# Performance work log

Hardware: AMD Instinct MI355X
Metric: run time of the kernel (lower is better)

Reference implementation:

```python
import jax, jax.numpy as jnp
import numpy as np

N = 25000      # nodes
E = 200000     # edges (avg degree 8)
DIN = 512      # input_dim
HID = 512      # hidden_dim


def setup_inputs() -> dict:
    key = jax.random.key(0)
    ks = jax.random.split(key, 8)
    x = jax.random.normal(ks[0], (N, DIN), jnp.float32)
    edge_index = jax.random.randint(ks[1], (2, E), 0, N, jnp.int32)
    s_in = 1.0 / np.sqrt(DIN).astype(np.float32)
    s_h = 1.0 / np.sqrt(HID).astype(np.float32)
    W1 = jax.random.normal(ks[2], (DIN, HID), jnp.float32) * s_in
    b1 = jnp.zeros((HID,), jnp.float32)
    W2 = jax.random.normal(ks[3], (HID, HID), jnp.float32) * s_h
    b2 = jnp.zeros((HID,), jnp.float32)
    Wo = jax.random.normal(ks[4], (HID, 1), jnp.float32) * s_h
    bo = jnp.zeros((1,), jnp.float32)
    Ww = jax.random.normal(ks[5], (HID, 1), jnp.float32) * s_h
    bw = jnp.zeros((1,), jnp.float32)
    return dict(x=x, edge_index=edge_index, W1=W1, b1=b1, W2=W2, b2=b2,
                Wo=Wo, bo=bo, Ww=Ww, bw=bw)


def reference(x, edge_index, W1, b1, W2, b2, Wo, bo, Ww, bw):
    n = x.shape[0]
    src, dst = edge_index[0], edge_index[1]
    # GCNConv with self-loops: deg counts incoming edges + 1 self-loop
    deg = jax.ops.segment_sum(jnp.ones(src.shape[0], x.dtype), dst,
                              num_segments=n) + 1.0
    dis = jax.lax.rsqrt(deg)              # deg^{-1/2}, [N]
    norm = dis[src] * dis[dst]            # per-edge symmetric norm, [E]

    def gcn(h, W, b):
        hw = h @ W                        # [N, H] dense GEMM
        msg = hw[src] * norm[:, None]     # gather + scale, [E, H]
        agg = jax.ops.segment_sum(msg, dst, num_segments=n)
        agg = agg + hw * (dis * dis)[:, None]  # self-loop contribution
        return agg + b

    h1 = jax.nn.relu(gcn(x, W1, b1))
    h2 = jax.nn.relu(gcn(h1, W2, b2))
    open_logits = (h2 @ Wo + bo)[:, 0]
    wall_logits = (h2 @ Ww + bw)[:, 0]
    return open_logits, wall_logits
```

## Files before the change

kernel.cpp:

```cpp
#include <hip/hip_runtime.h>
#include <hip/hip_bf16.h>

#define DIN 512
#define HID 512

#define AS1 __attribute__((address_space(1)))
#define AS3 __attribute__((address_space(3)))

typedef __attribute__((ext_vector_type(8))) short bfrag;
typedef __attribute__((ext_vector_type(4))) float ffrag;
typedef __attribute__((ext_vector_type(8))) unsigned short u16x8;
typedef __attribute__((ext_vector_type(4))) unsigned short u16x4;

__global__ __launch_bounds__(256) void prelude(const float* __restrict__ x,
                                               unsigned short* __restrict__ xb,
                                               const float* __restrict__ W1,
                                               const float* __restrict__ W2,
                                               unsigned short* __restrict__ Wt1,
                                               unsigned short* __restrict__ Wt2,
                                               const int* __restrict__ dst,
                                               int* __restrict__ cnt,
                                               int E, int Nvalid, int C1) {
    int b = blockIdx.x;
    if (b < C1) {
        int idx = b * 256 + threadIdx.x;
        int row = idx >> 6;
        int c = (idx & 63) * 8;
        unsigned short o[8];
        if (row < Nvalid) {
            float4 a = *(const float4*)&x[(size_t)row * 512 + c];
            float4 v = *(const float4*)&x[(size_t)row * 512 + c + 4];
            __hip_bfloat16 t;
            t = __float2bfloat16(a.x); o[0] = *(unsigned short*)&t;
            t = __float2bfloat16(a.y); o[1] = *(unsigned short*)&t;
            t = __float2bfloat16(a.z); o[2] = *(unsigned short*)&t;
            t = __float2bfloat16(a.w); o[3] = *(unsigned short*)&t;
            t = __float2bfloat16(v.x); o[4] = *(unsigned short*)&t;
            t = __float2bfloat16(v.y); o[5] = *(unsigned short*)&t;
            t = __float2bfloat16(v.z); o[6] = *(unsigned short*)&t;
            t = __float2bfloat16(v.w); o[7] = *(unsigned short*)&t;
        } else {
#pragma unroll
            for (int j = 0; j < 8; ++j) o[j] = 0;
        }
        *(u16x8*)&xb[(size_t)row * 512 + c] = *(u16x8*)o;
    } else if (b < C1 + 512) {
        int bb = b - C1;
        int which = bb >> 8;
        bb &= 255;
        const float* W = which ? W2 : W1;
        unsigned short* Wt = which ? Wt2 : Wt1;
        __shared__ float t[32][33];
        int tid = threadIdx.x;
        int tx = tid & 31, ty = tid >> 5;
        int n0 = (bb & 15) * 32, k0 = (bb >> 4) * 32;
#pragma unroll
        for (int s = 0; s < 4; ++s)
            t[ty + 8 * s][tx] = W[(size_t)(k0 + ty + 8 * s) * 512 + n0 + tx];
        __syncthreads();
#pragma unroll
        for (int s = 0; s < 4; ++s) {
            __hip_bfloat16 v = __float2bfloat16(t[tx][ty + 8 * s]);
            Wt[(size_t)(n0 + ty + 8 * s) * 512 + k0 + tx] = *(unsigned short*)&v;
        }
    } else {
        int e = (b - C1 - 512) * 256 + threadIdx.x;
        if (e < E) atomicAdd(&cnt[dst[e]], 1);
    }
}

__global__ __launch_bounds__(256) void scan1(const int* __restrict__ cnt, int* __restrict__ tmp,
                                             int* __restrict__ bsum, int N) {
    int tid = threadIdx.x, lane = tid & 63, wave = tid >> 6;
    int i = blockIdx.x * 256 + tid;
    int v = (i < N) ? cnt[i] : 0;
    int incl = v;
#pragma unroll
    for (int o = 1; o < 64; o <<= 1) {
        int t = __shfl_up(incl, o);
        if (lane >= o) incl += t;
    }
    __shared__ int wtot[4];
    if (lane == 63) wtot[wave] = incl;
    __syncthreads();
    int woff = 0;
#pragma unroll
    for (int w = 0; w < 4; ++w) woff += (w < wave) ? wtot[w] : 0;
    if (i < N) tmp[i] = woff + incl - v;
    if (tid == 255) bsum[blockIdx.x] = woff + incl;
}

__global__ void scan2(int* __restrict__ bsum, int nb) {
    int tid = threadIdx.x;
    int lane = tid & 63, wave = tid >> 6;
    int v = (tid < nb) ? bsum[tid] : 0;
    int incl = v;
#pragma unroll
    for (int o = 1; o < 64; o <<= 1) {
        int t = __shfl_up(incl, o);
        if (lane >= o) incl += t;
    }
    __shared__ int w0;
    if (tid == 63) w0 = incl;
    __syncthreads();
    int off = wave ? w0 : 0;
    if (tid < nb) bsum[tid] = off + incl - v;
    if (tid == 127) bsum[nb] = off + incl;
}

__global__ void scan3(const int* __restrict__ cnt, const int* __restrict__ tmp,
                      const int* __restrict__ bsum, int* __restrict__ offs,
                      int* __restrict__ cursor, float* __restrict__ dis,
                      float* __restrict__ out, const float* __restrict__ bo,
                      const float* __restrict__ bw, int N, int nb) {
    int i = blockIdx.x * 256 + threadIdx.x;
    if (i < N) {
        int o = tmp[i] + bsum[i >> 8];
        offs[i] = o;
        cursor[i] = o;
        dis[i] = rsqrtf((float)cnt[i] + 1.0f);
        out[i] = bo[0];
        out[N + i] = bw[0];
    }
    if (i == 0) offs[N] = bsum[nb];
}

__global__ void fill_kernel(const int* __restrict__ src, const int* __restrict__ dst,
                            int* __restrict__ cursor, const float* __restrict__ dis,
                            int2* __restrict__ csr2, int E) {
    int e = blockIdx.x * 256 + threadIdx.x;
    if (e >= E) return;
    int d = dst[e];
    int s = src[e];
    int pos = atomicAdd(&cursor[d], 1);
    int2 rec;
    rec.x = s;
    rec.y = __float_as_int(dis[s]);
    csr2[pos] = rec;
}

__device__ inline bool tile_map(int b, int Mtiles, int& m0, int& n0) {
    int xcd = b & 7, i = b >> 3;
    int nt = i & 3, mg = i >> 2;
    int mt = mg * 8 + xcd;
    if (mt >= Mtiles) return false;
    m0 = mt * 128;
    n0 = nt * 128;
    return true;
}

__global__ __launch_bounds__(256) void gemm_bf16(const short* __restrict__ A,
                                                 const short* __restrict__ B,
                                                 unsigned short* __restrict__ C,
                                                 int Mtiles) {
    __shared__ __align__(16) short As[128 * 64];
    __shared__ __align__(16) short Bs[128 * 64];
    const int K = 512;
    int m0, n0;
    if (!tile_map(blockIdx.x, Mtiles, m0, n0)) return;
    int tid = threadIdx.x;
    int lane = tid & 63, wave = tid >> 6;
    int wm = (wave & 1) * 64;
    int wn = (wave >> 1) * 64;
    int r = lane & 15, q = lane >> 4;

    unsigned aoff[4], boff[4]; int ldso[4];
#pragma unroll
    for (int i = 0; i < 4; ++i) {
        int s = i * 256 + tid;
        int row = s >> 3;
        int c = (s & 7) ^ (row & 7);
        aoff[i] = (unsigned)(m0 + row) * K + c * 8;
        boff[i] = (unsigned)(n0 + row) * K + c * 8;
        ldso[i] = (i * 256 + (tid & ~63)) * 8;
    }

    ffrag acc[4][4];
#pragma unroll
    for (int i = 0; i < 4; ++i)
#pragma unroll
        for (int j = 0; j < 4; ++j) acc[i][j] = ffrag{0.f, 0.f, 0.f, 0.f};

    for (int k0 = 0; k0 < K; k0 += 64) {
#pragma unroll
        for (int i = 0; i < 4; ++i) {
            __builtin_amdgcn_global_load_lds((const AS1 void*)(A + aoff[i] + k0),
                                             (AS3 void*)(As + ldso[i]), 16, 0, 0);
            __builtin_amdgcn_global_load_lds((const AS1 void*)(B + boff[i] + k0),
                                             (AS3 void*)(Bs + ldso[i]), 16, 0, 0);
        }
        __syncthreads();

#pragma unroll
        for (int s2 = 0; s2 < 2; ++s2) {
            bfrag af[4], bfr[4];
#pragma unroll
            for (int i = 0; i < 4; ++i) {
                int arow = wm + i * 16 + r;
                int ach = (s2 * 4 + q) ^ (arow & 7);
                af[i] = *(const bfrag*)&As[arow * 64 + ach * 8];
                int brow = wn + i * 16 + r;
                int bch = (s2 * 4 + q) ^ (brow & 7);
                bfr[i] = *(const bfrag*)&Bs[brow * 64 + bch * 8];
            }
#pragma unroll
            for (int i = 0; i < 4; ++i)
#pragma unroll
                for (int j = 0; j < 4; ++j)
                    acc[i][j] = __builtin_amdgcn_mfma_f32_16x16x32_bf16(bfr[j], af[i], acc[i][j], 0, 0, 0);
        }
        __syncthreads();
    }

#pragma unroll
    for (int i = 0; i < 4; ++i) {
        int m = m0 + wm + i * 16 + r;
#pragma unroll
        for (int j = 0; j < 4; ++j) {
            int n = n0 + wn + j * 16 + q * 4;
            u16x4 o;
#pragma unroll
            for (int reg = 0; reg < 4; ++reg) {
                __hip_bfloat16 v = __float2bfloat16(acc[i][j][reg]);
                o[reg] = *(unsigned short*)&v;
            }
            *(u16x4*)&C[(size_t)m * 512 + n] = o;
        }
    }
}

__device__ inline void cvt8(u16x8 v, float* f) {
#pragma unroll
    for (int j = 0; j < 8; ++j) f[j] = __uint_as_float((unsigned)v[j] << 16);
}

__global__ __launch_bounds__(256) void agg_relu_sh(const unsigned short* __restrict__ hw,
                                                   const int2* __restrict__ csr2,
                                                   const int* __restrict__ offs,
                                                   const float* __restrict__ dis,
                                                   const float* __restrict__ bias,
                                                   unsigned short* __restrict__ out,
                                                   int N, int Mpad) {
    int b = blockIdx.x;
    int shard = b & 7;
    int tid = threadIdx.x;
    int wave = tid >> 6, lane = tid & 63;
    int cluster = lane >> 3;
    int sub = lane & 7;
    int node = (b >> 3) * 32 + wave * 8 + cluster;
    int c0 = shard * 64 + sub * 8;
    if (node >= N) {
        if (node < Mpad) {
            u16x8 z = {0, 0, 0, 0, 0, 0, 0, 0};
            *(u16x8*)&out[(size_t)node * HID + c0] = z;
        }
        return;
    }

    float dn = dis[node];
    int e0 = offs[node], e1 = offs[node + 1];

    float acc[8];
    {
        u16x8 sv = *(const u16x8*)&hw[(size_t)node * HID + c0];
        float g[8];
        cvt8(sv, g);
        float4 bb0 = *(const float4*)&bias[c0];
        float4 bb1 = *(const float4*)&bias[c0 + 4];
        float dis2 = dn * dn;
        acc[0] = g[0] * dis2 + bb0.x; acc[1] = g[1] * dis2 + bb0.y;
        acc[2] = g[2] * dis2 + bb0.z; acc[3] = g[3] * dis2 + bb0.w;
        acc[4] = g[4] * dis2 + bb1.x; acc[5] = g[5] * dis2 + bb1.y;
        acc[6] = g[6] * dis2 + bb1.z; acc[7] = g[7] * dis2 + bb1.w;
    }

    for (int e = e0; e < e1; e += 4) {
        int idx[4]; float wgt[4];
#pragma unroll
        for (int j = 0; j < 4; ++j) {
            int ee = e + j;
            int ec = (ee < e1) ? ee : (e1 - 1);
            int2 rec = csr2[ec];
            idx[j] = rec.x;
            wgt[j] = (ee < e1) ? __int_as_float(rec.y) * dn : 0.f;
        }
        u16x8 v[4];
#pragma unroll
        for (int j = 0; j < 4; ++j)
            v[j] = *(const u16x8*)&hw[(size_t)idx[j] * HID + c0];
#pragma unroll
        for (int j = 0; j < 4; ++j) {
            float g[8];
            cvt8(v[j], g);
#pragma unroll
            for (int t = 0; t < 8; ++t) acc[t] += g[t] * wgt[j];
        }
    }

    unsigned short o[8];
#pragma unroll
    for (int j = 0; j < 8; ++j) {
        __hip_bfloat16 v = __float2bfloat16(fmaxf(acc[j], 0.f));
        o[j] = *(unsigned short*)&v;
    }
    *(u16x8*)&out[(size_t)node * HID + c0] = *(u16x8*)o;
}

__global__ __launch_bounds__(256) void agg_heads_sh(const unsigned short* __restrict__ hw,
                                                    const int2* __restrict__ csr2,
                                                    const int* __restrict__ offs,
                                                    const float* __restrict__ dis,
                                                    const float* __restrict__ bias,
                                                    const float* __restrict__ Wo,
                                                    const float* __restrict__ Ww,
                                                    float* __restrict__ out, int N) {
    int b = blockIdx.x;
    int shard = b & 7;
    int tid = threadIdx.x;
    int wave = tid >> 6, lane = tid & 63;
    int cluster = lane >> 3;
    int sub = lane & 7;
    int node = (b >> 3) * 32 + wave * 8 + cluster;
    if (node >= N) return;
    int c0 = shard * 64 + sub * 8;

    float dn = dis[node];
    int e0 = offs[node], e1 = offs[node + 1];

    float acc[8];
    {
        u16x8 sv = *(const u16x8*)&hw[(size_t)node * HID + c0];
        float g[8];
        cvt8(sv, g);
        float4 bb0 = *(const float4*)&bias[c0];
        float4 bb1 = *(const float4*)&bias[c0 + 4];
        float dis2 = dn * dn;
        acc[0] = g[0] * dis2 + bb0.x; acc[1] = g[1] * dis2 + bb0.y;
        acc[2] = g[2] * dis2 + bb0.z; acc[3] = g[3] * dis2 + bb0.w;
        acc[4] = g[4] * dis2 + bb1.x; acc[5] = g[5] * dis2 + bb1.y;
        acc[6] = g[6] * dis2 + bb1.z; acc[7] = g[7] * dis2 + bb1.w;
    }

    for (int e = e0; e < e1; e += 4) {
        int idx[4]; float wgt[4];
#pragma unroll
        for (int j = 0; j < 4; ++j) {
            int ee = e + j;
            int ec = (ee < e1) ? ee : (e1 - 1);
            int2 rec = csr2[ec];
            idx[j] = rec.x;
            wgt[j] = (ee < e1) ? __int_as_float(rec.y) * dn : 0.f;
        }
        u16x8 v[4];
#pragma unroll
        for (int j = 0; j < 4; ++j)
            v[j] = *(const u16x8*)&hw[(size_t)idx[j] * HID + c0];
#pragma unroll
        for (int j = 0; j < 4; ++j) {
            float g[8];
            cvt8(v[j], g);
#pragma unroll
            for (int t = 0; t < 8; ++t) acc[t] += g[t] * wgt[j];
        }
    }

    float4 wo0 = *(const float4*)&Wo[c0];
    float4 wo1 = *(const float4*)&Wo[c0 + 4];
    float4 ww0 = *(const float4*)&Ww[c0];
    float4 ww1 = *(const float4*)&Ww[c0 + 4];
    float po = 0.f, pw = 0.f, h;
    h = fmaxf(acc[0], 0.f); po += h * wo0.x; pw += h * ww0.x;
    h = fmaxf(acc[1], 0.f); po += h * wo0.y; pw += h * ww0.y;
    h = fmaxf(acc[2], 0.f); po += h * wo0.z; pw += h * ww0.z;
    h = fmaxf(acc[3], 0.f); po += h * wo0.w; pw += h * ww0.w;
    h = fmaxf(acc[4], 0.f); po += h * wo1.x; pw += h * ww1.x;
    h = fmaxf(acc[5], 0.f); po += h * wo1.y; pw += h * ww1.y;
    h = fmaxf(acc[6], 0.f); po += h * wo1.z; pw += h * ww1.z;
    h = fmaxf(acc[7], 0.f); po += h * wo1.w; pw += h * ww1.w;

#pragma unroll
    for (int off = 4; off > 0; off >>= 1) {
        po += __shfl_down(po, off);
        pw += __shfl_down(pw, off);
    }
    if (sub == 0) {
        atomicAdd(&out[node], po);
        atomicAdd(&out[N + node], pw);
    }
}

extern "C" void kernel_launch(void* const* d_in, const int* in_sizes, int n_in,
                              void* d_out, int out_size, void* d_ws, size_t ws_size,
                              hipStream_t stream) {
    const float* x  = (const float*)d_in[0];
    const int*   ei = (const int*)d_in[1];
    const float* W1 = (const float*)d_in[2];
    const float* b1 = (const float*)d_in[3];
    const float* W2 = (const float*)d_in[4];
    const float* b2 = (const float*)d_in[5];
    const float* Wo = (const float*)d_in[6];
    const float* bo = (const float*)d_in[7];
    const float* Ww = (const float*)d_in[8];
    const float* bw = (const float*)d_in[9];

    const int N = in_sizes[0] / DIN;
    const int E = in_sizes[1] / 2;
    const int Mpad = (N + 127) & ~127;
    const int Mtiles = Mpad / 128;
    const int nb = (N + 255) / 256;
    const int C1 = Mpad / 4;

    char* ws = (char*)d_ws;
    size_t p = 0;
    auto alloc = [&](size_t bytes) -> char* {
        char* r = ws + p;
        p += (bytes + 255) & ~(size_t)255;
        return r;
    };
    int*   cnt    = (int*)alloc((size_t)N * 4);
    int*   offs   = (int*)alloc((size_t)(N + 1) * 4);
    int*   cursor = (int*)alloc((size_t)N * 4);
    int*   tmp    = (int*)alloc((size_t)N * 4);
    int*   bsum   = (int*)alloc(132 * 4);
    float* dis    = (float*)alloc((size_t)N * 4);
    int2*  csr2   = (int2*)alloc((size_t)E * 8 + 64);
    unsigned short* xb  = (unsigned short*)alloc((size_t)Mpad * 512 * 2);
    unsigned short* Wt1 = (unsigned short*)alloc((size_t)512 * 512 * 2);
    unsigned short* Wt2 = (unsigned short*)alloc((size_t)512 * 512 * 2);
    unsigned short* hw  = (unsigned short*)alloc((size_t)Mpad * 512 * 2);
    unsigned short* h1  = (unsigned short*)alloc((size_t)Mpad * 512 * 2);

    const int* src = ei;
    const int* dst = ei + E;

    hipMemsetAsync(cnt, 0, (size_t)N * 4, stream);

    prelude<<<C1 + 512 + (E + 255) / 256, 256, 0, stream>>>(x, xb, W1, W2, Wt1, Wt2,
                                                            dst, cnt, E, N, C1);
    scan1<<<nb, 256, 0, stream>>>(cnt, tmp, bsum, N);
    scan2<<<1, 128, 0, stream>>>(bsum, nb);
    scan3<<<nb, 256, 0, stream>>>(cnt, tmp, bsum, offs, cursor, dis,
                                  (float*)d_out, bo, bw, N, nb);
    fill_kernel<<<(E + 255) / 256, 256, 0, stream>>>(src, dst, cursor, dis, csr2, E);

    const int ggrid = 8 * ((Mtiles + 7) / 8) * 4;
    gemm_bf16<<<ggrid, 256, 0, stream>>>((const short*)xb, (const short*)Wt1, hw, Mtiles);
    agg_relu_sh<<<8 * (Mpad / 32), 256, 0, stream>>>(hw, csr2, offs, dis, b1, h1, N, Mpad);
    gemm_bf16<<<ggrid, 256, 0, stream>>>((const short*)h1, (const short*)Wt2, hw, Mtiles);
    agg_heads_sh<<<8 * ((N + 31) / 32), 256, 0, stream>>>(hw, csr2, offs, dis, b2,
                                                          Wo, Ww, (float*)d_out, N);
}
```

Measured before the change: 247.2 us.

## Replace prefix scan with atomic offset assignment and degree-sorted node permutation

Drops the three-kernel prefix scan. Each node now takes its CSR offset from a single global atomic counter, so segments are no longer laid out in node order, and segment ends come from the degree rather than offs[node+1]. It also bucket-sorts nodes by degree into a permutation, so the aggregation kernels process nodes of similar degree together and the 8 nodes in a wave see less load imbalance. The costs are heavy contention on one global atomic, less locality in the CSR layout, and indirect node indexing through perm in the aggregation kernels.

```diff
diff --git a/kernel.cpp b/kernel.cpp
--- a/kernel.cpp
+++ b/kernel.cpp
@@ -69,74 +69,62 @@
     }
 }
 
-__global__ __launch_bounds__(256) void scan1(const int* __restrict__ cnt, int* __restrict__ tmp,
-                                             int* __restrict__ bsum, int N) {
-    int tid = threadIdx.x, lane = tid & 63, wave = tid >> 6;
-    int i = blockIdx.x * 256 + tid;
-    int v = (i < N) ? cnt[i] : 0;
-    int incl = v;
-#pragma unroll
-    for (int o = 1; o < 64; o <<= 1) {
-        int t = __shfl_up(incl, o);
-        if (lane >= o) incl += t;
-    }
-    __shared__ int wtot[4];
-    if (lane == 63) wtot[wave] = incl;
-    __syncthreads();
-    int woff = 0;
-#pragma unroll
-    for (int w = 0; w < 4; ++w) woff += (w < wave) ? wtot[w] : 0;
-    if (i < N) tmp[i] = woff + incl - v;
-    if (tid == 255) bsum[blockIdx.x] = woff + incl;
-}
-
-__global__ void scan2(int* __restrict__ bsum, int nb) {
-    int tid = threadIdx.x;
-    int lane = tid & 63, wave = tid >> 6;
-    int v = (tid < nb) ? bsum[tid] : 0;
-    int incl = v;
-#pragma unroll
-    for (int o = 1; o < 64; o <<= 1) {
-        int t = __shfl_up(incl, o);
-        if (lane >= o) incl += t;
-    }
-    __shared__ int w0;
-    if (tid == 63) w0 = incl;
-    __syncthreads();
-    int off = wave ? w0 : 0;
-    if (tid < nb) bsum[tid] = off + incl - v;
-    if (tid == 127) bsum[nb] = off + incl;
-}
-
-__global__ void scan3(const int* __restrict__ cnt, const int* __restrict__ tmp,
-                      const int* __restrict__ bsum, int* __restrict__ offs,
-                      int* __restrict__ cursor, float* __restrict__ dis,
-                      float* __restrict__ out, const float* __restrict__ bo,
-                      const float* __restrict__ bw, int N, int nb) {
+__global__ __launch_bounds__(256) void assign(int* __restrict__ cnt,
+                                              int* __restrict__ offs,
+                                              int* __restrict__ cursor,
+                                              float* __restrict__ dis,
+                                              float* __restrict__ out,
+                                              const float* __restrict__ bo,
+                                              const float* __restrict__ bw,
+                                              int N) {
+    int* bcnt = cnt + N;
+    int* gctr = cnt + N + 128;
     int i = blockIdx.x * 256 + threadIdx.x;
-    if (i < N) {
-        int o = tmp[i] + bsum[i >> 8];
-        offs[i] = o;
-        cursor[i] = o;
-        dis[i] = rsqrtf((float)cnt[i] + 1.0f);
-        out[i] = bo[0];
-        out[N + i] = bw[0];
-    }
-    if (i == 0) offs[N] = bsum[nb];
-}
-
-__global__ void fill_kernel(const int* __restrict__ src, const int* __restrict__ dst,
-                            int* __restrict__ cursor, const float* __restrict__ dis,
-                            int2* __restrict__ csr2, int E) {
-    int e = blockIdx.x * 256 + threadIdx.x;
-    if (e >= E) return;
-    int d = dst[e];
-    int s = src[e];
-    int pos = atomicAdd(&cursor[d], 1);
-    int2 rec;
-    rec.x = s;
-    rec.y = __float_as_int(dis[s]);
-    csr2[pos] = rec;
+    if (i >= N) return;
+    int d = cnt[i];
+    int o = atomicAdd(gctr, d);
+    offs[i] = o;
+    cursor[i] = o;
+    dis[i] = rsqrtf((float)d + 1.0f);
+    out[i] = bo[0];
+    out[N + i] = bw[0];
+    int b = (d < 63) ? d : 63;
+    atomicAdd(&bcnt[b], 1);
+}
+
+__global__ __launch_bounds__(256) void fill2(const int* __restrict__ src,
+                                             const int* __restrict__ dst,
+                                             int* __restrict__ cursor,
+                                             const float* __restrict__ dis,
+                                             int2* __restrict__ csr2,
+                                             int* __restrict__ cnt,
+                                             int* __restrict__ perm,
+                                             int E, int N, int EJ) {
+    int b = blockIdx.x;
+    if (b < EJ) {
+        int e = b * 256 + threadIdx.x;
+        if (e >= E) return;
+        int d = dst[e];
+        int s = src[e];
+        int pos = atomicAdd(&cursor[d], 1);
+        int2 rec;
+        rec.x = s;
+        rec.y = __float_as_int(dis[s]);
+        csr2[pos] = rec;
+    } else {
+        const int* bcnt = cnt + N;
+        int* bcur = cnt + N + 64;
+        int i = (b - EJ) * 256 + threadIdx.x;
+        if (i >= N) return;
+        int d = cnt[i];
+        int myb = (d < 63) ? d : 63;
+        int base = 0;
+#pragma unroll
+        for (int k = 0; k < 63; ++k)
+            base += (k < myb) ? bcnt[k] : 0;
+        int p = atomicAdd(&bcur[myb], 1);
+        perm[base + p] = i;
+    }
 }
 
 __device__ inline bool tile_map(int b, int Mtiles, int& m0, int& n0) {
@@ -237,8 +225,10 @@
 __global__ __launch_bounds__(256) void agg_relu_sh(const unsigned short* __restrict__ hw,
                                                    const int2* __restrict__ csr2,
                                                    const int* __restrict__ offs,
+                                                   const int* __restrict__ deg,
                                                    const float* __restrict__ dis,
                                                    const float* __restrict__ bias,
+                                                   const int* __restrict__ perm,
                                                    unsigned short* __restrict__ out,
                                                    int N, int Mpad) {
     int b = blockIdx.x;
@@ -247,18 +237,19 @@
     int wave = tid >> 6, lane = tid & 63;
     int cluster = lane >> 3;
     int sub = lane & 7;
-    int node = (b >> 3) * 32 + wave * 8 + cluster;
+    int j = (b >> 3) * 32 + wave * 8 + cluster;
     int c0 = shard * 64 + sub * 8;
-    if (node >= N) {
-        if (node < Mpad) {
+    if (j >= N) {
+        if (j < Mpad) {
             u16x8 z = {0, 0, 0, 0, 0, 0, 0, 0};
-            *(u16x8*)&out[(size_t)node * HID + c0] = z;
+            *(u16x8*)&out[(size_t)j * HID + c0] = z;
         }
         return;
     }
+    int node = perm[j];
 
     float dn = dis[node];
-    int e0 = offs[node], e1 = offs[node + 1];
+    int e0 = offs[node], e1 = e0 + deg[node];
 
     float acc[8];
     {
@@ -277,31 +268,31 @@
     for (int e = e0; e < e1; e += 4) {
         int idx[4]; float wgt[4];
 #pragma unroll
-        for (int j = 0; j < 4; ++j) {
-            int ee = e + j;
+        for (int t = 0; t < 4; ++t) {
+            int ee = e + t;
             int ec = (ee < e1) ? ee : (e1 - 1);
             int2 rec = csr2[ec];
-            idx[j] = rec.x;
-            wgt[j] = (ee < e1) ? __int_as_float(rec.y) * dn : 0.f;
+            idx[t] = rec.x;
+            wgt[t] = (ee < e1) ? __int_as_float(rec.y) * dn : 0.f;
         }
         u16x8 v[4];
 #pragma unroll
-        for (int j = 0; j < 4; ++j)
-            v[j] = *(const u16x8*)&hw[(size_t)idx[j] * HID + c0];
-#pragma unroll
-        for (int j = 0; j < 4; ++j) {
+        for (int t = 0; t < 4; ++t)
+            v[t] = *(const u16x8*)&hw[(size_t)idx[t] * HID + c0];
+#pragma unroll
+        for (int t = 0; t < 4; ++t) {
             float g[8];
-            cvt8(v[j], g);
-#pragma unroll
-            for (int t = 0; t < 8; ++t) acc[t] += g[t] * wgt[j];
+            cvt8(v[t], g);
+#pragma unroll
+            for (int u = 0; u < 8; ++u) acc[u] += g[u] * wgt[t];
         }
     }
 
     unsigned short o[8];
 #pragma unroll
-    for (int j = 0; j < 8; ++j) {
-        __hip_bfloat16 v = __float2bfloat16(fmaxf(acc[j], 0.f));
-        o[j] = *(unsigned short*)&v;
+    for (int t = 0; t < 8; ++t) {
+        __hip_bfloat16 v = __float2bfloat16(fmaxf(acc[t], 0.f));
+        o[t] = *(unsigned short*)&v;
     }
     *(u16x8*)&out[(size_t)node * HID + c0] = *(u16x8*)o;
 }
@@ -309,10 +300,12 @@
 __global__ __launch_bounds__(256) void agg_heads_sh(const unsigned short* __restrict__ hw,
                                                     const int2* __restrict__ csr2,
                                                     const int* __restrict__ offs,
+                                                    const int* __restrict__ deg,
                                                     const float* __restrict__ dis,
                                                     const float* __restrict__ bias,
                                                     const float* __restrict__ Wo,
                                                     const float* __restrict__ Ww,
+                                                    const int* __restrict__ perm,
                                                     float* __restrict__ out, int N) {
     int b = blockIdx.x;
     int shard = b & 7;
@@ -320,12 +313,13 @@
     int wave = tid >> 6, lane = tid & 63;
     int cluster = lane >> 3;
     int sub = lane & 7;
-    int node = (b >> 3) * 32 + wave * 8 + cluster;
-    if (node >= N) return;
+    int j = (b >> 3) * 32 + wave * 8 + cluster;
+    if (j >= N) return;
+    int node = perm[j];
     int c0 = shard * 64 + sub * 8;
 
     float dn = dis[node];
-    int e0 = offs[node], e1 = offs[node + 1];
+    int e0 = offs[node], e1 = e0 + deg[node];
 
     float acc[8];
     {
@@ -344,23 +338,23 @@
     for (int e = e0; e < e1; e += 4) {
         int idx[4]; float wgt[4];
 #pragma unroll
-        for (int j = 0; j < 4; ++j) {
-            int ee = e + j;
+        for (int t = 0; t < 4; ++t) {
+            int ee = e + t;
             int ec = (ee < e1) ? ee : (e1 - 1);
             int2 rec = csr2[ec];
-            idx[j] = rec.x;
-            wgt[j] = (ee < e1) ? __int_as_float(rec.y) * dn : 0.f;
+            idx[t] = rec.x;
+            wgt[t] = (ee < e1) ? __int_as_float(rec.y) * dn : 0.f;
         }
         u16x8 v[4];
 #pragma unroll
-        for (int j = 0; j < 4; ++j)
-            v[j] = *(const u16x8*)&hw[(size_t)idx[j] * HID + c0];
-#pragma unroll
-        for (int j = 0; j < 4; ++j) {
+        for (int t = 0; t < 4; ++t)
+            v[t] = *(const u16x8*)&hw[(size_t)idx[t] * HID + c0];
+#pragma unroll
+        for (int t = 0; t < 4; ++t) {
             float g[8];
-            cvt8(v[j], g);
-#pragma unroll
-            for (int t = 0; t < 8; ++t) acc[t] += g[t] * wgt[j];
+            cvt8(v[t], g);
+#pragma unroll
+            for (int u = 0; u < 8; ++u) acc[u] += g[u] * wgt[t];
         }
     }
 
@@ -409,6 +403,7 @@
     const int Mtiles = Mpad / 128;
     const int nb = (N + 255) / 256;
     const int C1 = Mpad / 4;
+    const int EJ = (E + 255) / 256;
 
     char* ws = (char*)d_ws;
     size_t p = 0;
@@ -417,11 +412,10 @@
         p += (bytes + 255) & ~(size_t)255;
         return r;
     };
-    int*   cnt    = (int*)alloc((size_t)N * 4);
-    int*   offs   = (int*)alloc((size_t)(N + 1) * 4);
+    int*   cnt    = (int*)alloc((size_t)(N + 132) * 4);
+    int*   offs   = (int*)alloc((size_t)N * 4);
     int*   cursor = (int*)alloc((size_t)N * 4);
-    int*   tmp    = (int*)alloc((size_t)N * 4);
-    int*   bsum   = (int*)alloc(132 * 4);
+    int*   perm   = (int*)alloc((size_t)N * 4);
     float* dis    = (float*)alloc((size_t)N * 4);
     int2*  csr2   = (int2*)alloc((size_t)E * 8 + 64);
     unsigned short* xb  = (unsigned short*)alloc((size_t)Mpad * 512 * 2);
@@ -433,20 +427,20 @@
     const int* src = ei;
     const int* dst = ei + E;
 
-    hipMemsetAsync(cnt, 0, (size_t)N * 4, stream);
-
-    prelude<<<C1 + 512 + (E + 255) / 256, 256, 0, stream>>>(x, xb, W1, W2, Wt1, Wt2,
-                                                            dst, cnt, E, N, C1);
-    scan1<<<nb, 256, 0, stream>>>(cnt, tmp, bsum, N);
-    scan2<<<1, 128, 0, stream>>>(bsum, nb);
-    scan3<<<nb, 256, 0, stream>>>(cnt, tmp, bsum, offs, cursor, dis,
-                                  (float*)d_out, bo, bw, N, nb);
-    fill_kernel<<<(E + 255) / 256, 256, 0, stream>>>(src, dst, cursor, dis, csr2, E);
+    hipMemsetAsync(cnt, 0, (size_t)(N + 132) * 4, stream);
+
+    prelude<<<C1 + 512 + EJ, 256, 0, stream>>>(x, xb, W1, W2, Wt1, Wt2,
+                                               dst, cnt, E, N, C1);
+    assign<<<nb, 256, 0, stream>>>(cnt, offs, cursor, dis,
+                                   (float*)d_out, bo, bw, N);
+    fill2<<<EJ + nb, 256, 0, stream>>>(src, dst, cursor, dis, csr2, cnt, perm,
+                                       E, N, EJ);
 
     const int ggrid = 8 * ((Mtiles + 7) / 8) * 4;
     gemm_bf16<<<ggrid, 256, 0, stream>>>((const short*)xb, (const short*)Wt1, hw, Mtiles);
-    agg_relu_sh<<<8 * (Mpad / 32), 256, 0, stream>>>(hw, csr2, offs, dis, b1, h1, N, Mpad);
+    agg_relu_sh<<<8 * (Mpad / 32), 256, 0, stream>>>(hw, csr2, offs, cnt, dis, b1,
+                                                     perm, h1, N, Mpad);
     gemm_bf16<<<ggrid, 256, 0, stream>>>((const short*)h1, (const short*)Wt2, hw, Mtiles);
-    agg_heads_sh<<<8 * ((N + 31) / 32), 256, 0, stream>>>(hw, csr2, offs, dis, b2,
-                                                          Wo, Ww, (float*)d_out, N);
-}
+    agg_heads_sh<<<8 * ((N + 31) / 32), 256, 0, stream>>>(hw, csr2, offs, cnt, dis, b2,
+                                                          Wo, Ww, perm, (float*)d_out, N);
+}
```

Result: slower. 398.2 us (+61.1%).
